# Kernel optimization log

Measured on AMD Instinct MI355X. Metric: run time of the kernel, lower is better.

## Reference

```python
import jax, jax.numpy as jnp
import numpy as np

MIN_NORM = 1e-15
EPS = 1e-7          # fp32 eps used by hgcn Hyperboloid
MAX_NORM = 1e6
C = 1.0             # curvature for all layers (args.c = 1)
N, D = 16384, 64

# ---- Hyperboloid manifold ops (faithful to hgcn manifolds/hyperboloid.py) ----

def _norm(v):
    return jnp.sqrt(jnp.sum(v * v, axis=-1, keepdims=True))

def proj(x, c):
    K = 1.0 / c
    y = x[..., 1:]
    x0 = jnp.sqrt(jnp.clip(K + jnp.sum(y * y, -1, keepdims=True), EPS))
    return jnp.concatenate([x0, y], -1)

def proj_tan0(u, c):
    return jnp.concatenate([jnp.zeros_like(u[..., :1]), u[..., 1:]], -1)

def expmap0(u, c):
    sqrtK = (1.0 / c) ** 0.5
    x = u[..., 1:]
    xn = jnp.clip(_norm(x), MIN_NORM)
    theta = xn / sqrtK
    res = jnp.concatenate([sqrtK * jnp.cosh(theta),
                           sqrtK * jnp.sinh(theta) * x / xn], -1)
    return proj(res, c)

def logmap0(x, c):
    sqrtK = (1.0 / c) ** 0.5
    y = x[..., 1:]
    yn = jnp.clip(_norm(y), MIN_NORM)
    theta = jnp.clip(x[..., :1] / sqrtK, 1.0 + EPS)
    return jnp.concatenate([jnp.zeros_like(theta),
                            sqrtK * jnp.arccosh(theta) * y / yn], -1)

def mink_dot(x, y):
    return -x[..., :1] * y[..., :1] + jnp.sum(x[..., 1:] * y[..., 1:], -1, keepdims=True)

def expmap(u, x, c):
    sqrtK = (1.0 / c) ** 0.5
    normu = jnp.minimum(jnp.sqrt(jnp.clip(mink_dot(u, u), EPS)), MAX_NORM)
    theta = jnp.clip(normu / sqrtK, MIN_NORM)
    return proj(jnp.cosh(theta) * x + jnp.sinh(theta) * u / theta, c)

def proj_tan(u, x, c):
    ux = jnp.sum(x[..., 1:] * u[..., 1:], -1, keepdims=True)
    return jnp.concatenate([ux / jnp.clip(x[..., :1], EPS), u[..., 1:]], -1)

def ptransp0(x, u, c):
    sqrtK = (1.0 / c) ** 0.5
    x0, y = x[..., :1], x[..., 1:]
    yn = jnp.clip(_norm(y), MIN_NORM)
    yhat = y / yn
    v = jnp.concatenate([-yn, (sqrtK - x0) * yhat], -1)
    alpha = jnp.sum(yhat * u[..., 1:], -1, keepdims=True) / sqrtK
    return proj_tan(u - alpha * v, x, c)

def mobius_add(x, y, c):
    u = logmap0(y, c)
    v = ptransp0(x, u, c)
    return expmap(v, x, c)

# ---- HGCN layers (HypLinear -> HypAgg -> HypAct), dropout=0, use_att=False ----

def hyp_linear(x, W, b, c):
    mv = expmap0(logmap0(x, c) @ W.T, c)   # mobius_matvec
    res = proj(mv, c)
    hyp_bias = proj(expmap0(proj_tan0(b[None, :], c), c), c)
    return proj(mobius_add(res, hyp_bias, c), c)

def hyp_agg(x, adj_n, c):
    return proj(expmap0(adj_n @ logmap0(x, c), c), c)

def hyp_act(x, c_in, c_out):
    xt = proj_tan0(jax.nn.relu(logmap0(x, c_in)), c_out)
    return proj(expmap0(xt, c_out), c_out)

def hgc_layer(x, adj_n, W, b, c_in, c_out):
    h = hyp_linear(x, W, b, c_in)
    h = hyp_agg(h, adj_n, c_in)
    return hyp_act(h, c_in, c_out)

def setup_inputs() -> dict:
    key = jax.random.key(0)
    k1, k2, k3, k4, k5, k6 = jax.random.split(key, 6)
    return {
        "x": jax.random.normal(k1, (N, D), jnp.float32),
        "adj": jax.random.uniform(k2, (N, N), jnp.float32),
        "W1": jax.random.normal(k3, (D, D), jnp.float32) * 0.125,
        "b1": jax.random.normal(k4, (D,), jnp.float32) * 0.01,
        "W2": jax.random.normal(k5, (D, D), jnp.float32) * 0.125,
        "b2": jax.random.normal(k6, (D,), jnp.float32) * 0.01,
    }

def reference(x, adj, W1, b1, W2, b2):
    # project input to hyperboloid
    x_hyp = proj(expmap0(proj_tan0(x, C), C), C)
    # row-normalize adjacency: D^{-1} A (inf -> 0)
    rsum = jnp.sum(adj, axis=1)
    rinv = jnp.where(rsum != 0, 1.0 / rsum, 0.0)
    adj_n = rinv[:, None] * adj
    h1 = hgc_layer(x_hyp, adj_n, W1, b1, C, C)
    h2 = hgc_layer(h1, adj_n, W2, b2, C, C)
    return (h1, h2)
```

## Files before the change

### kernel.cpp

```cpp
#include <hip/hip_runtime.h>
#include <cstdint>
#include <cstddef>

#define NROWS 16384
#define KDIM  16384
#define EPSF  1e-7f
#define MINN  1e-15f
#define MAXN  1e6f
#define KSPLIT 4
#define KRANGE (KDIM/KSPLIT)
#define BM    64
#define BK    64
#define NSTEP (KRANGE/BK)
#define PG    1040
#define ABUF  (8*PG)

typedef __attribute__((ext_vector_type(8)))  short short8;
typedef __attribute__((ext_vector_type(4)))  float f32x4;
typedef __attribute__((ext_vector_type(16))) float f32x16;

__device__ __forceinline__ short f2bf(float f){
  union { float f; unsigned u; } c; c.f = f;
  unsigned u = c.u;
  unsigned r = (u + 0x7FFFu + ((u >> 16) & 1u)) >> 16;
  return (short)r;
}

__device__ __forceinline__ float wredsum(float v){
  v += __shfl_xor(v, 1);
  v += __shfl_xor(v, 2);
  v += __shfl_xor(v, 4);
  v += __shfl_xor(v, 8);
  v += __shfl_xor(v, 16);
  v += __shfl_xor(v, 32);
  return v;
}

__global__ __launch_bounds__(128) void k_bias(const float* __restrict__ b1,
                                              const float* __restrict__ b2,
                                              float* __restrict__ ub){
  int w = threadIdx.x >> 6, l = threadIdx.x & 63;
  const float* b = w ? b2 : b1;
  float bv = b[l];
  float tb = l ? bv : 0.f;
  float s  = wredsum(tb*tb);
  float xn = fmaxf(sqrtf(s), MINN);
  float sc = sinhf(xn)/xn;
  float e  = sc*tb;
  float s2 = wredsum(e*e);
  float x0 = sqrtf(fmaxf(1.f+s2, EPSF));
  float yn = fmaxf(sqrtf(s2), MINN);
  float th = fmaxf(x0, 1.f+EPSF);
  float u  = l ? acoshf(th)*e/yn : 0.f;
  ub[w*64 + l] = u;
}

template<int MODE>
__global__ __launch_bounds__(256) void k_linear(const float* __restrict__ in,
                                                const float* __restrict__ W,
                                                const float* __restrict__ ub,
                                                float* __restrict__ g){
  __shared__ float Wt[64*65];
  int tid = threadIdx.x;
  for(int idx = tid; idx < 4096; idx += 256){
    int j = idx >> 6, k = idx & 63;
    Wt[k*65 + j] = W[idx];
  }
  __syncthreads();
  int lane = tid & 63;
  int row  = blockIdx.x*4 + (tid >> 6);
  float v = in[(size_t)row*64 + lane];
  float lx;
  if (MODE == 0){
    float t  = lane ? v : 0.f;
    float s  = wredsum(t*t);
    float tn = fmaxf(sqrtf(s), MINN);
    float sc = sinhf(tn)/tn;
    float e  = sc*t;
    float s2 = wredsum(e*e);
    float x0 = sqrtf(fmaxf(1.f+s2, EPSF));
    float yn = fmaxf(sqrtf(s2), MINN);
    float th = fmaxf(x0, 1.f+EPSF);
    lx = lane ? acoshf(th)*e/yn : 0.f;
  } else {
    float t  = lane ? v : 0.f;
    float s2 = wredsum(t*t);
    float x0 = __shfl(v, 0);
    float yn = fmaxf(sqrtf(s2), MINN);
    float th = fmaxf(x0, 1.f+EPSF);
    lx = lane ? acoshf(th)*t/yn : 0.f;
  }
  float mv = 0.f;
  #pragma unroll
  for(int k = 0; k < 64; k++){
    mv = fmaf(__shfl(lx, k), Wt[k*65 + lane], mv);
  }
  float u  = lane ? mv : 0.f;
  float s  = wredsum(u*u);
  float un = fmaxf(sqrtf(s), MINN);
  float sc = sinhf(un)/un;
  float e  = sc*u;
  float s2 = wredsum(e*e);
  float r0 = sqrtf(fmaxf(1.f+s2, EPSF));
  float ubt   = lane ? ub[lane] : 0.f;
  float yn    = fmaxf(sqrtf(s2), MINN);
  float yhat  = e/yn;
  float alpha = wredsum(yhat*ubt);
  float w     = ubt - alpha*(1.f - r0)*yhat;
  float ux    = wredsum(e*w);
  float v0    = ux / fmaxf(r0, EPSF);
  float md    = wredsum(w*w) - v0*v0;
  float normu = fminf(sqrtf(fmaxf(md, EPSF)), MAXN);
  float th2   = fmaxf(normu, MINN);
  float ch    = coshf(th2);
  float shq   = sinhf(th2)/th2;
  float ov    = ch*(lane ? e : r0) + shq*(lane ? w : v0);
  float ot    = lane ? ov : 0.f;
  float s3    = wredsum(ot*ot);
  float o0    = sqrtf(fmaxf(1.f+s3, EPSF));
  float yn2 = fmaxf(sqrtf(s3), MINN);
  float th3 = fmaxf(o0, 1.f+EPSF);
  float gv  = lane ? acoshf(th3)*ot/yn2 : 0.f;
  g[(size_t)row*64 + lane] = gv;
}

__global__ __launch_bounds__(256) void k_tr(const float* __restrict__ g,
                                            short* __restrict__ gT){
  __shared__ float t[64][65];
  int tid = threadIdx.x;
  int b   = blockIdx.x;
  int r   = tid >> 2;
  int c0  = (tid & 3)*16;
  const float* src = g + ((size_t)b*64 + r)*64 + c0;
  #pragma unroll
  for(int i = 0; i < 4; i++){
    float4 v = *(const float4*)(src + i*4);
    t[r][c0 + i*4 + 0] = v.x; t[r][c0 + i*4 + 1] = v.y;
    t[r][c0 + i*4 + 2] = v.z; t[r][c0 + i*4 + 3] = v.w;
  }
  __syncthreads();
  int n   = tid >> 2;
  int seg = tid & 3;
  short8 p0, p1;
  #pragma unroll
  for(int j = 0; j < 8; j++) p0[j] = f2bf(t[seg*16 + j][n]);
  #pragma unroll
  for(int j = 0; j < 8; j++) p1[j] = f2bf(t[seg*16 + 8 + j][n]);
  short* dst = gT + (size_t)n*KDIM + b*64 + seg*16;
  *(short8*)(dst)     = p0;
  *(short8*)(dst + 8) = p1;
}

template<bool FIRST>
__global__ __launch_bounds__(256, 4) void k_matmul(const float* __restrict__ adj,
                                                   const short* __restrict__ gT,
                                                   float* __restrict__ pagg,
                                                   float* __restrict__ prsum){
  __shared__ __align__(16) char Alds[2*ABUF];
  int tid  = threadIdx.x;
  int lane = tid & 63, w = tid >> 6;
  int rb   = blockIdx.x;
  int ks   = blockIdx.y;
  int row0 = rb*BM;
  size_t k0 = (size_t)ks * KRANGE;

  int sr   = tid >> 2;
  int sseg = tid & 3;
  const float4* ap = (const float4*)(adj + (size_t)(row0 + sr)*KDIM + k0 + sseg*16);
  int AwOff0 = (sseg*2)*PG   + sr*16;
  int AwOff1 = (sseg*2+1)*PG + sr*16;

  int wm = w >> 1, wn = w & 1;
  int lr = lane & 31, lh = lane >> 5;
  int ArdOff = lh*PG + (wm*32 + lr)*16;
  const short* bp = gT + (size_t)(wn*32 + lr)*KDIM + k0 + lh*8;

  f32x16 acc;
  #pragma unroll
  for(int q = 0; q < 16; q++) acc[q] = 0.f;
  float rs = 0.f;

  float4 aR[4], aN[4];
  short8 bC[4], bN[4];

  #pragma unroll
  for(int q = 0; q < 4; q++) aR[q] = ap[q];
  {
    if (FIRST){
      #pragma unroll
      for(int q = 0; q < 4; q++) rs += aR[q].x + aR[q].y + aR[q].z + aR[q].w;
    }
    short8 lo = { f2bf(aR[0].x), f2bf(aR[0].y), f2bf(aR[0].z), f2bf(aR[0].w),
                  f2bf(aR[1].x), f2bf(aR[1].y), f2bf(aR[1].z), f2bf(aR[1].w) };
    short8 hi = { f2bf(aR[2].x), f2bf(aR[2].y), f2bf(aR[2].z), f2bf(aR[2].w),
                  f2bf(aR[3].x), f2bf(aR[3].y), f2bf(aR[3].z), f2bf(aR[3].w) };
    *(short8*)(Alds + AwOff0) = lo;
    *(short8*)(Alds + AwOff1) = hi;
  }
  #pragma unroll
  for(int q = 0; q < 4; q++) aR[q] = ap[16 + q];
  #pragma unroll
  for(int c = 0; c < 4; c++) bC[c] = *(const short8*)(bp + c*16);
  __syncthreads();

  for (int i = 0; i < NSTEP; i++){
    const char* Ab = Alds + (i & 1)*ABUF;
    short8 af0 = *(const short8*)(Ab + ArdOff);
    short8 af1 = *(const short8*)(Ab + ArdOff + 2*PG);
    short8 af2 = *(const short8*)(Ab + ArdOff + 4*PG);
    short8 af3 = *(const short8*)(Ab + ArdOff + 6*PG);
    if (i + 2 < NSTEP){
      #pragma unroll
      for(int q = 0; q < 4; q++) aN[q] = ap[(i+2)*16 + q];
    }
    if (i + 1 < NSTEP){
      #pragma unroll
      for(int c = 0; c < 4; c++) bN[c] = *(const short8*)(bp + (size_t)(i+1)*BK + c*16);
    }
    acc = __builtin_amdgcn_mfma_f32_32x32x16_bf16(af0, bC[0], acc, 0, 0, 0);
    acc = __builtin_amdgcn_mfma_f32_32x32x16_bf16(af1, bC[1], acc, 0, 0, 0);
    acc = __builtin_amdgcn_mfma_f32_32x32x16_bf16(af2, bC[2], acc, 0, 0, 0);
    acc = __builtin_amdgcn_mfma_f32_32x32x16_bf16(af3, bC[3], acc, 0, 0, 0);
    if (i + 1 < NSTEP){
      char* Aw = Alds + ((i+1) & 1)*ABUF;
      if (FIRST){
        #pragma unroll
        for(int q = 0; q < 4; q++) rs += aR[q].x + aR[q].y + aR[q].z + aR[q].w;
      }
      short8 lo = { f2bf(aR[0].x), f2bf(aR[0].y), f2bf(aR[0].z), f2bf(aR[0].w),
                    f2bf(aR[1].x), f2bf(aR[1].y), f2bf(aR[1].z), f2bf(aR[1].w) };
      short8 hi = { f2bf(aR[2].x), f2bf(aR[2].y), f2bf(aR[2].z), f2bf(aR[2].w),
                    f2bf(aR[3].x), f2bf(aR[3].y), f2bf(aR[3].z), f2bf(aR[3].w) };
      *(short8*)(Aw + AwOff0) = lo;
      *(short8*)(Aw + AwOff1) = hi;
    }
    #pragma unroll
    for(int q = 0; q < 4; q++) aR[q] = aN[q];
    #pragma unroll
    for(int c = 0; c < 4; c++) bC[c] = bN[c];
    __syncthreads();
  }

  if (FIRST){
    rs += __shfl_xor(rs, 1);
    rs += __shfl_xor(rs, 2);
    if ((tid & 3) == 0) prsum[(size_t)ks*NROWS + row0 + sr] = rs;
  }
  float* ob = pagg + ((size_t)ks*NROWS + row0 + wm*32)*64 + wn*32;
  #pragma unroll
  for(int q = 0; q < 16; q++){
    int rl = (q & 3) + 8*(q >> 2) + 4*lh;
    ob[(size_t)rl*64 + lr] = acc[q];
  }
}

template<int LAYER>
__global__ __launch_bounds__(256) void k_post(const float* __restrict__ pagg,
                                              const float* __restrict__ prsum,
                                              float* __restrict__ rinv,
                                              float* __restrict__ h){
  int tid = threadIdx.x; int lane = tid & 63;
  int row = blockIdx.x*4 + (tid >> 6);
  float s = 0.f;
  #pragma unroll
  for(int ks = 0; ks < KSPLIT; ks++) s += pagg[(size_t)ks*NROWS*64 + (size_t)row*64 + lane];
  float ri;
  if (LAYER == 1){
    float rsum = 0.f;
    #pragma unroll
    for(int ks = 0; ks < KSPLIT; ks++) rsum += prsum[(size_t)ks*NROWS + row];
    ri = (rsum != 0.f) ? 1.f/rsum : 0.f;
    if (lane == 0) rinv[row] = ri;
  } else {
    ri = rinv[row];
  }
  float a  = s * ri;
  float at = lane ? a : 0.f;
  float ss = wredsum(at*at);
  float un = fmaxf(sqrtf(ss), MINN);
  float sc = sinhf(un)/un;
  float e  = sc*at;
  float s2 = wredsum(e*e);
  float x0 = sqrtf(fmaxf(1.f+s2, EPSF));
  float yn = fmaxf(sqrtf(s2), MINN);
  float th = fmaxf(x0, 1.f+EPSF);
  float lt = lane ? acoshf(th)*e/yn : 0.f;
  float rl = fmaxf(lt, 0.f);
  float s3 = wredsum(rl*rl);
  float rn = fmaxf(sqrtf(s3), MINN);
  float sc2= sinhf(rn)/rn;
  float e2 = sc2*rl;
  float s4 = wredsum(e2*e2);
  float h0 = sqrtf(fmaxf(1.f+s4, EPSF));
  h[(size_t)row*64 + lane] = lane ? e2 : h0;
}

extern "C" void kernel_launch(void* const* d_in, const int* in_sizes, int n_in,
                              void* d_out, int out_size, void* d_ws, size_t ws_size,
                              hipStream_t stream){
  const float* x   = (const float*)d_in[0];
  const float* adj = (const float*)d_in[1];
  const float* W1  = (const float*)d_in[2];
  const float* b1  = (const float*)d_in[3];
  const float* W2  = (const float*)d_in[4];
  const float* b2  = (const float*)d_in[5];
  float* out = (float*)d_out;
  float* h1  = out;
  float* h2  = out + (size_t)NROWS*64;

  float* wsf   = (float*)d_ws;
  float* gbuf  = wsf;
  float* pagg  = gbuf  + (size_t)NROWS*64;
  float* prsum = pagg  + (size_t)KSPLIT*NROWS*64;
  float* rinv  = prsum + (size_t)KSPLIT*NROWS;
  float* ubs   = rinv  + NROWS;
  short* gT    = (short*)(ubs + 128);

  dim3 gm(NROWS/BM, KSPLIT);

  k_bias<<<1, 128, 0, stream>>>(b1, b2, ubs);
  k_linear<0><<<NROWS/4, 256, 0, stream>>>(x, W1, ubs, gbuf);
  k_tr<<<NROWS/64, 256, 0, stream>>>(gbuf, gT);
  k_matmul<true><<<gm, 256, 0, stream>>>(adj, gT, pagg, prsum);
  k_post<1><<<NROWS/4, 256, 0, stream>>>(pagg, prsum, rinv, h1);
  k_linear<1><<<NROWS/4, 256, 0, stream>>>(h1, W2, ubs + 64, gbuf);
  k_tr<<<NROWS/64, 256, 0, stream>>>(gbuf, gT);
  k_matmul<false><<<gm, 256, 0, stream>>>(adj, gT, pagg, prsum);
  k_post<2><<<NROWS/4, 256, 0, stream>>>(pagg, prsum, rinv, h2);
}
```

Before: 597.4 us.

## Convert adjacency to FP8 once and run both aggregations with FP8 MFMA

Adds a pass that reads the fp32 adjacency once, computes row sums and reciprocals, and writes an FP8 copy. Both aggregation matmuls then stream this 1-byte copy with fp8 MFMA instead of re-reading fp32 and converting to bf16 inside the loop. The features are also packed to FP8, and KSPLIT doubles to keep enough blocks in flight. This cuts adjacency traffic in the second layer but adds a full conversion pass, and FP8 precision on adjacency and features may hurt accuracy.

```diff
diff --git a/kernel.cpp b/kernel.cpp
--- a/kernel.cpp
+++ b/kernel.cpp
@@ -7,24 +7,18 @@
 #define EPSF  1e-7f
 #define MINN  1e-15f
 #define MAXN  1e6f
-#define KSPLIT 4
+#define KSPLIT 8
 #define KRANGE (KDIM/KSPLIT)
 #define BM    64
 #define BK    64
 #define NSTEP (KRANGE/BK)
-#define PG    1040
+#define PG    528
 #define ABUF  (8*PG)
 
-typedef __attribute__((ext_vector_type(8)))  short short8;
-typedef __attribute__((ext_vector_type(4)))  float f32x4;
 typedef __attribute__((ext_vector_type(16))) float f32x16;
-
-__device__ __forceinline__ short f2bf(float f){
-  union { float f; unsigned u; } c; c.f = f;
-  unsigned u = c.u;
-  unsigned r = (u + 0x7FFFu + ((u >> 16) & 1u)) >> 16;
-  return (short)r;
-}
+typedef long long i64;
+typedef unsigned long long u64;
+typedef unsigned int uint;
 
 __device__ __forceinline__ float wredsum(float v){
   v += __shfl_xor(v, 1);
@@ -53,6 +47,30 @@
   float th = fmaxf(x0, 1.f+EPSF);
   float u  = l ? acoshf(th)*e/yn : 0.f;
   ub[w*64 + l] = u;
+}
+
+__global__ __launch_bounds__(256) void k_cvt(const float* __restrict__ adj,
+                                             uint* __restrict__ adjF8,
+                                             float* __restrict__ rinv){
+  int tid = threadIdx.x;
+  int r   = tid >> 5;
+  int l32 = tid & 31;
+  int row = blockIdx.x*8 + r;
+  const float4* src = (const float4*)(adj + (size_t)row*KDIM);
+  uint* dst = adjF8 + (size_t)row*(KDIM/4);
+  float rs = 0.f;
+  #pragma unroll 4
+  for(int it = 0; it < KDIM/128; it++){
+    float4 v = src[it*32 + l32];
+    rs += (v.x + v.y) + (v.z + v.w);
+    uint p = __builtin_amdgcn_cvt_pk_fp8_f32(v.x, v.y, 0u, false);
+    p = __builtin_amdgcn_cvt_pk_fp8_f32(v.z, v.w, p, true);
+    dst[it*32 + l32] = p;
+  }
+  rs += __shfl_xor(rs, 1);  rs += __shfl_xor(rs, 2);
+  rs += __shfl_xor(rs, 4);  rs += __shfl_xor(rs, 8);
+  rs += __shfl_xor(rs, 16);
+  if (l32 == 0) rinv[row] = (rs != 0.f) ? 1.f/rs : 0.f;
 }
 
 template<int MODE>
@@ -124,8 +142,8 @@
   g[(size_t)row*64 + lane] = gv;
 }
 
-__global__ __launch_bounds__(256) void k_tr(const float* __restrict__ g,
-                                            short* __restrict__ gT){
+__global__ __launch_bounds__(256) void k_trf8(const float* __restrict__ g,
+                                              uint* __restrict__ gF8T){
   __shared__ float t[64][65];
   int tid = threadIdx.x;
   int b   = blockIdx.x;
@@ -141,21 +159,23 @@
   __syncthreads();
   int n   = tid >> 2;
   int seg = tid & 3;
-  short8 p0, p1;
-  #pragma unroll
-  for(int j = 0; j < 8; j++) p0[j] = f2bf(t[seg*16 + j][n]);
-  #pragma unroll
-  for(int j = 0; j < 8; j++) p1[j] = f2bf(t[seg*16 + 8 + j][n]);
-  short* dst = gT + (size_t)n*KDIM + b*64 + seg*16;
-  *(short8*)(dst)     = p0;
-  *(short8*)(dst + 8) = p1;
-}
-
-template<bool FIRST>
-__global__ __launch_bounds__(256, 4) void k_matmul(const float* __restrict__ adj,
-                                                   const short* __restrict__ gT,
-                                                   float* __restrict__ pagg,
-                                                   float* __restrict__ prsum){
+  int s16 = seg*16;
+  uint4 p;
+  p.x = __builtin_amdgcn_cvt_pk_fp8_f32(t[s16+ 0][n], t[s16+ 1][n], 0u, false);
+  p.x = __builtin_amdgcn_cvt_pk_fp8_f32(t[s16+ 2][n], t[s16+ 3][n], p.x, true);
+  p.y = __builtin_amdgcn_cvt_pk_fp8_f32(t[s16+ 4][n], t[s16+ 5][n], 0u, false);
+  p.y = __builtin_amdgcn_cvt_pk_fp8_f32(t[s16+ 6][n], t[s16+ 7][n], p.y, true);
+  p.z = __builtin_amdgcn_cvt_pk_fp8_f32(t[s16+ 8][n], t[s16+ 9][n], 0u, false);
+  p.z = __builtin_amdgcn_cvt_pk_fp8_f32(t[s16+10][n], t[s16+11][n], p.z, true);
+  p.w = __builtin_amdgcn_cvt_pk_fp8_f32(t[s16+12][n], t[s16+13][n], 0u, false);
+  p.w = __builtin_amdgcn_cvt_pk_fp8_f32(t[s16+14][n], t[s16+15][n], p.w, true);
+  uint4* dst = (uint4*)gF8T + (size_t)n*(KDIM/16) + b*4 + seg;
+  *dst = p;
+}
+
+__global__ __launch_bounds__(256) void k_matmul(const unsigned char* __restrict__ adjF8,
+                                                const unsigned char* __restrict__ gF8T,
+                                                float* __restrict__ pagg){
   __shared__ __align__(16) char Alds[2*ABUF];
   int tid  = threadIdx.x;
   int lane = tid & 63, w = tid >> 6;
@@ -166,86 +186,60 @@
 
   int sr   = tid >> 2;
   int sseg = tid & 3;
-  const float4* ap = (const float4*)(adj + (size_t)(row0 + sr)*KDIM + k0 + sseg*16);
-  int AwOff0 = (sseg*2)*PG   + sr*16;
-  int AwOff1 = (sseg*2+1)*PG + sr*16;
+  const uint4* ap = (const uint4*)(adjF8 + (size_t)(row0 + sr)*KDIM + k0 + sseg*16);
+  int AwOff0 = (2*sseg    )*PG + sr*8;
+  int AwOff1 = (2*sseg + 1)*PG + sr*8;
 
   int wm = w >> 1, wn = w & 1;
   int lr = lane & 31, lh = lane >> 5;
-  int ArdOff = lh*PG + (wm*32 + lr)*16;
-  const short* bp = gT + (size_t)(wn*32 + lr)*KDIM + k0 + lh*8;
+  int ArdOff = lh*PG + (wm*32 + lr)*8;
+  const unsigned char* bp = gF8T + (size_t)(wn*32 + lr)*KDIM + k0 + lh*8;
 
   f32x16 acc;
   #pragma unroll
   for(int q = 0; q < 16; q++) acc[q] = 0.f;
-  float rs = 0.f;
-
-  float4 aR[4], aN[4];
-  short8 bC[4], bN[4];
-
-  #pragma unroll
-  for(int q = 0; q < 4; q++) aR[q] = ap[q];
+
+  uint4 aR, aN;
+  i64 bC[4], bN[4];
+
+  aR = ap[0];
   {
-    if (FIRST){
-      #pragma unroll
-      for(int q = 0; q < 4; q++) rs += aR[q].x + aR[q].y + aR[q].z + aR[q].w;
-    }
-    short8 lo = { f2bf(aR[0].x), f2bf(aR[0].y), f2bf(aR[0].z), f2bf(aR[0].w),
-                  f2bf(aR[1].x), f2bf(aR[1].y), f2bf(aR[1].z), f2bf(aR[1].w) };
-    short8 hi = { f2bf(aR[2].x), f2bf(aR[2].y), f2bf(aR[2].z), f2bf(aR[2].w),
-                  f2bf(aR[3].x), f2bf(aR[3].y), f2bf(aR[3].z), f2bf(aR[3].w) };
-    *(short8*)(Alds + AwOff0) = lo;
-    *(short8*)(Alds + AwOff1) = hi;
-  }
-  #pragma unroll
-  for(int q = 0; q < 4; q++) aR[q] = ap[16 + q];
-  #pragma unroll
-  for(int c = 0; c < 4; c++) bC[c] = *(const short8*)(bp + c*16);
+    union { uint4 v; u64 q[2]; } u; u.v = aR;
+    *(u64*)(Alds + AwOff0) = u.q[0];
+    *(u64*)(Alds + AwOff1) = u.q[1];
+  }
+  aR = ap[4];
+  #pragma unroll
+  for(int m = 0; m < 4; m++) bC[m] = *(const i64*)(bp + m*16);
   __syncthreads();
 
   for (int i = 0; i < NSTEP; i++){
     const char* Ab = Alds + (i & 1)*ABUF;
-    short8 af0 = *(const short8*)(Ab + ArdOff);
-    short8 af1 = *(const short8*)(Ab + ArdOff + 2*PG);
-    short8 af2 = *(const short8*)(Ab + ArdOff + 4*PG);
-    short8 af3 = *(const short8*)(Ab + ArdOff + 6*PG);
-    if (i + 2 < NSTEP){
-      #pragma unroll
-      for(int q = 0; q < 4; q++) aN[q] = ap[(i+2)*16 + q];
-    }
+    i64 af0 = *(const i64*)(Ab + ArdOff);
+    i64 af1 = *(const i64*)(Ab + ArdOff + 2*PG);
+    i64 af2 = *(const i64*)(Ab + ArdOff + 4*PG);
+    i64 af3 = *(const i64*)(Ab + ArdOff + 6*PG);
+    if (i + 2 < NSTEP) aN = ap[(i+2)*4];
     if (i + 1 < NSTEP){
       #pragma unroll
-      for(int c = 0; c < 4; c++) bN[c] = *(const short8*)(bp + (size_t)(i+1)*BK + c*16);
+      for(int m = 0; m < 4; m++) bN[m] = *(const i64*)(bp + (size_t)(i+1)*BK + m*16);
     }
-    acc = __builtin_amdgcn_mfma_f32_32x32x16_bf16(af0, bC[0], acc, 0, 0, 0);
-    acc = __builtin_amdgcn_mfma_f32_32x32x16_bf16(af1, bC[1], acc, 0, 0, 0);
-    acc = __builtin_amdgcn_mfma_f32_32x32x16_bf16(af2, bC[2], acc, 0, 0, 0);
-    acc = __builtin_amdgcn_mfma_f32_32x32x16_bf16(af3, bC[3], acc, 0, 0, 0);
+    acc = __builtin_amdgcn_mfma_f32_32x32x16_fp8_fp8(af0, bC[0], acc, 0, 0, 0);
+    acc = __builtin_amdgcn_mfma_f32_32x32x16_fp8_fp8(af1, bC[1], acc, 0, 0, 0);
+    acc = __builtin_amdgcn_mfma_f32_32x32x16_fp8_fp8(af2, bC[2], acc, 0, 0, 0);
+    acc = __builtin_amdgcn_mfma_f32_32x32x16_fp8_fp8(af3, bC[3], acc, 0, 0, 0);
     if (i + 1 < NSTEP){
       char* Aw = Alds + ((i+1) & 1)*ABUF;
-      if (FIRST){
-        #pragma unroll
-        for(int q = 0; q < 4; q++) rs += aR[q].x + aR[q].y + aR[q].z + aR[q].w;
-      }
-      short8 lo = { f2bf(aR[0].x), f2bf(aR[0].y), f2bf(aR[0].z), f2bf(aR[0].w),
-                    f2bf(aR[1].x), f2bf(aR[1].y), f2bf(aR[1].z), f2bf(aR[1].w) };
-      short8 hi = { f2bf(aR[2].x), f2bf(aR[2].y), f2bf(aR[2].z), f2bf(aR[2].w),
-                    f2bf(aR[3].x), f2bf(aR[3].y), f2bf(aR[3].z), f2bf(aR[3].w) };
-      *(short8*)(Aw + AwOff0) = lo;
-      *(short8*)(Aw + AwOff1) = hi;
+      union { uint4 v; u64 q[2]; } u; u.v = aR;
+      *(u64*)(Aw + AwOff0) = u.q[0];
+      *(u64*)(Aw + AwOff1) = u.q[1];
     }
+    aR = aN;
     #pragma unroll
-    for(int q = 0; q < 4; q++) aR[q] = aN[q];
-    #pragma unroll
-    for(int c = 0; c < 4; c++) bC[c] = bN[c];
+    for(int m = 0; m < 4; m++) bC[m] = bN[m];
     __syncthreads();
   }
 
-  if (FIRST){
-    rs += __shfl_xor(rs, 1);
-    rs += __shfl_xor(rs, 2);
-    if ((tid & 3) == 0) prsum[(size_t)ks*NROWS + row0 + sr] = rs;
-  }
   float* ob = pagg + ((size_t)ks*NROWS + row0 + wm*32)*64 + wn*32;
   #pragma unroll
   for(int q = 0; q < 16; q++){
@@ -254,27 +248,15 @@
   }
 }
 
-template<int LAYER>
 __global__ __launch_bounds__(256) void k_post(const float* __restrict__ pagg,
-                                              const float* __restrict__ prsum,
-                                              float* __restrict__ rinv,
+                                              const float* __restrict__ rinv,
                                               float* __restrict__ h){
   int tid = threadIdx.x; int lane = tid & 63;
   int row = blockIdx.x*4 + (tid >> 6);
   float s = 0.f;
   #pragma unroll
   for(int ks = 0; ks < KSPLIT; ks++) s += pagg[(size_t)ks*NROWS*64 + (size_t)row*64 + lane];
-  float ri;
-  if (LAYER == 1){
-    float rsum = 0.f;
-    #pragma unroll
-    for(int ks = 0; ks < KSPLIT; ks++) rsum += prsum[(size_t)ks*NROWS + row];
-    ri = (rsum != 0.f) ? 1.f/rsum : 0.f;
-    if (lane == 0) rinv[row] = ri;
-  } else {
-    ri = rinv[row];
-  }
-  float a  = s * ri;
+  float a  = s * rinv[row];
   float at = lane ? a : 0.f;
   float ss = wredsum(at*at);
   float un = fmaxf(sqrtf(ss), MINN);
@@ -311,20 +293,21 @@
   float* wsf   = (float*)d_ws;
   float* gbuf  = wsf;
   float* pagg  = gbuf  + (size_t)NROWS*64;
-  float* prsum = pagg  + (size_t)KSPLIT*NROWS*64;
-  float* rinv  = prsum + (size_t)KSPLIT*NROWS;
+  float* rinv  = pagg  + (size_t)KSPLIT*NROWS*64;
   float* ubs   = rinv  + NROWS;
-  short* gT    = (short*)(ubs + 128);
+  uint*  gF8T  = (uint*)(ubs + 128);
+  uint*  adjF8 = gF8T + (size_t)64*KDIM/4;
 
   dim3 gm(NROWS/BM, KSPLIT);
 
   k_bias<<<1, 128, 0, stream>>>(b1, b2, ubs);
+  k_cvt<<<NROWS/8, 256, 0, stream>>>(adj, adjF8, rinv);
   k_linear<0><<<NROWS/4, 256, 0, stream>>>(x, W1, ubs, gbuf);
-  k_tr<<<NROWS/64, 256, 0, stream>>>(gbuf, gT);
-  k_matmul<true><<<gm, 256, 0, stream>>>(adj, gT, pagg, prsum);
-  k_post<1><<<NROWS/4, 256, 0, stream>>>(pagg, prsum, rinv, h1);
+  k_trf8<<<NROWS/64, 256, 0, stream>>>(gbuf, gF8T);
+  k_matmul<<<gm, 256, 0, stream>>>((const unsigned char*)adjF8, (const unsigned char*)gF8T, pagg);
+  k_post<<<NROWS/4, 256, 0, stream>>>(pagg, rinv, h1);
   k_linear<1><<<NROWS/4, 256, 0, stream>>>(h1, W2, ubs + 64, gbuf);
-  k_tr<<<NROWS/64, 256, 0, stream>>>(gbuf, gT);
-  k_matmul<false><<<gm, 256, 0, stream>>>(adj, gT, pagg, prsum);
-  k_post<2><<<NROWS/4, 256, 0, stream>>>(pagg, prsum, rinv, h2);
-}
+  k_trf8<<<NROWS/64, 256, 0, stream>>>(gbuf, gF8T);
+  k_matmul<<<gm, 256, 0, stream>>>((const unsigned char*)adjF8, (const unsigned char*)gF8T, pagg);
+  k_post<<<NROWS/4, 256, 0, stream>>>(pagg, rinv, h2);
+}
```

New measurement: 640.4 us. 7.2% more time.
